# Performance work log

Hardware: AMD Instinct MI355X
Metric: run time of the kernel (lower is better)

## Reference

```python
import jax, jax.numpy as jnp
import numpy as np

B, S, D, H, DH, N, L, VOCAB = 8, 512, 1024, 16, 64, 32, 2, 128

def _ln(x, g, b, eps=1e-5):
    m = jnp.mean(x, axis=-1, keepdims=True)
    v = jnp.var(x, axis=-1, keepdims=True)
    return (x - m) * jax.lax.rsqrt(v + eps) * g + b

def setup_inputs() -> dict:
    key = jax.random.key(0)
    ks = jax.random.split(key, 10)
    std = 0.02
    inp = {
        "tokens": jax.random.randint(ks[0], (B, S), 0, VOCAB),
        "emb": jax.random.normal(ks[1], (VOCAB, D), jnp.float32) * std,
        "pos": jax.random.normal(ks[2], (1, S, D), jnp.float32) * std,
        "ln_g": jnp.ones((L, D), jnp.float32),
        "ln_b": jnp.zeros((L, D), jnp.float32),
        "wq": jax.random.normal(ks[3], (L, D, D), jnp.float32) * std,
        "bq": jnp.zeros((L, D), jnp.float32),
        "wk": jax.random.normal(ks[4], (L, D, D), jnp.float32) * std,
        "bk": jnp.zeros((L, D), jnp.float32),
        "wv": jax.random.normal(ks[5], (L, D, D), jnp.float32) * std,
        "bv": jnp.zeros((L, D), jnp.float32),
        "wg": jax.random.normal(ks[6], (L, D, D), jnp.float32) * std,
        "bg": jnp.zeros((L, D), jnp.float32),
        "wo": jax.random.normal(ks[7], (L, D, D), jnp.float32) * std,
        "bo": jnp.zeros((L, D), jnp.float32),
        "alpha_logit": jax.random.normal(ks[8], (L, H, N), jnp.float32) * 0.1,
        "fn_g": jnp.ones((D,), jnp.float32),
        "fn_b": jnp.zeros((D,), jnp.float32),
        "head_w": jax.random.normal(ks[9], (VOCAB, D), jnp.float32) * std,
        "head_b": jnp.zeros((VOCAB,), jnp.float32),
    }
    return inp

def _layer(x, g, b, Wq, Bq, Wk, Bk, Wv, Bv, Wg, Bg, Wo, Bo, alogit):
    residual = x
    xn = _ln(x, g, b)  # (B,S,D)
    def proj(W, Bb):
        return (jnp.einsum('bsd,ed->bse', xn, W) + Bb).reshape(x.shape[0], x.shape[1], H, DH)
    Q, K, V = proj(Wq, Bq), proj(Wk, Bk), proj(Wv, Bv)
    gate = jax.nn.silu(proj(Wg, Bg))
    alpha = jax.nn.sigmoid(alogit)  # (H,N)
    # scan over time; carry h: (B,H,N,DH)
    h0 = jnp.zeros((x.shape[0], H, N, DH), x.dtype)
    qkv = (jnp.moveaxis(Q, 1, 0), jnp.moveaxis(K, 1, 0), jnp.moveaxis(V, 1, 0))  # (S,B,H,DH)
    def step(h, qkv_t):
        q_t, k_t, v_t = qkv_t
        k_state = k_t[:, :, :N]  # state_dim <= d_head
        h = alpha[None, :, :, None] * h + jnp.einsum('bhi,bhj->bhij', k_state, v_t)
        q_state = q_t[:, :, :N]
        o_t = jnp.einsum('bhi,bhij->bhj', q_state, h)
        return h, o_t
    _, O = jax.lax.scan(step, h0, qkv)  # O: (S,B,H,DH)
    o = jnp.moveaxis(O, 0, 1) * gate  # (B,S,H,DH)
    o = o.reshape(x.shape[0], x.shape[1], H * DH)
    y = jnp.einsum('bsd,ed->bse', o, Wo) + Bo
    return residual + y

def reference(tokens, emb, pos, ln_g, ln_b, wq, bq, wk, bk, wv, bv, wg, bg, wo, bo,
              alpha_logit, fn_g, fn_b, head_w, head_b):
    x = emb[tokens] + pos[:, :tokens.shape[1], :]
    for l in range(L):
        x = _layer(x, ln_g[l], ln_b[l], wq[l], bq[l], wk[l], bk[l], wv[l], bv[l],
                   wg[l], bg[l], wo[l], bo[l], alpha_logit[l])
    x = _ln(x, fn_g, fn_b)
    logits = jnp.einsum('bsd,vd->bsv', x, head_w) + head_b
    return logits
```

## Files before the change

kernel.cpp:

```cpp
#include <hip/hip_runtime.h>
#include <hip/hip_bf16.h>
#include <stdint.h>

#define D_MODEL 1024
#define BB 8
#define SS 512
#define HH 16
#define DHH 64
#define NN 32
#define LL 2
#define VOC 128
#define M_TOK (BB * SS)
#define CHUNK 32
#define NCHUNK 16

typedef __bf16 bf16x8_t __attribute__((ext_vector_type(8)));
typedef float floatx4_t __attribute__((ext_vector_type(4)));
typedef unsigned short u16;

__device__ __forceinline__ float b2f(u16 u) {
  union { unsigned int i; float f; } c; c.i = ((unsigned int)u) << 16; return c.f;
}
__device__ __forceinline__ u16 f2b(float f) {
  union { float f; unsigned int i; } c; c.f = f;
  unsigned int r = c.i + 0x7fffu + ((c.i >> 16) & 1u);
  return (u16)(r >> 16);
}
__device__ __forceinline__ float sigm(float x) {
  return 1.0f / (1.0f + __expf(-x));
}

#define WSEG 524288
#define HSEG 32768
struct SrcP { const float* p[6]; };
__global__ __launch_bounds__(256) void k_f2b_all(
    SrcP src, u16* __restrict__ dst) {
  int i = blockIdx.x * 256 + threadIdx.x;
  int seg, within;
  if (i < 5 * WSEG) { seg = i / WSEG; within = i - seg * WSEG; }
  else { seg = 5; within = i - 5 * WSEG; if (within >= HSEG) return; }
  float4 v = ((const float4*)src.p[seg])[within];
  ushort4 o;
  o.x = f2b(v.x); o.y = f2b(v.y); o.z = f2b(v.z); o.w = f2b(v.w);
  ((ushort4*)dst)[(size_t)seg * WSEG + within] = o;
}

__global__ __launch_bounds__(256) void k_embed_ln(
    const int* __restrict__ tok, const float* __restrict__ emb,
    const float* __restrict__ pos, const float* __restrict__ g,
    const float* __restrict__ b, float* __restrict__ x, u16* __restrict__ xn) {
  int m = blockIdx.x;
  int s = m & (SS - 1);
  int tkn = tok[m];
  int t = threadIdx.x;
  int d = t * 4;
  float4 ev = *(const float4*)&emb[(size_t)tkn * D_MODEL + d];
  float4 pv = *(const float4*)&pos[(size_t)s * D_MODEL + d];
  float4 v;
  v.x = ev.x + pv.x; v.y = ev.y + pv.y; v.z = ev.z + pv.z; v.w = ev.w + pv.w;
  *(float4*)&x[(size_t)m * D_MODEL + d] = v;

  float s1 = v.x + v.y + v.z + v.w;
  float s2 = v.x * v.x + v.y * v.y + v.z * v.z + v.w * v.w;
#pragma unroll
  for (int o = 1; o < 64; o <<= 1) {
    s1 += __shfl_xor(s1, o);
    s2 += __shfl_xor(s2, o);
  }
  __shared__ float red[8];
  int wv = t >> 6, lane = t & 63;
  if (lane == 0) { red[wv] = s1; red[4 + wv] = s2; }
  __syncthreads();
  s1 = red[0] + red[1] + red[2] + red[3];
  s2 = red[4] + red[5] + red[6] + red[7];
  float mean = s1 * (1.0f / D_MODEL);
  float var = s2 * (1.0f / D_MODEL) - mean * mean;
  float rstd = rsqrtf(var + 1e-5f);
  float4 gv = *(const float4*)&g[d];
  float4 bv = *(const float4*)&b[d];
  ushort4 ov;
  ov.x = f2b((v.x - mean) * rstd * gv.x + bv.x);
  ov.y = f2b((v.y - mean) * rstd * gv.y + bv.y);
  ov.z = f2b((v.z - mean) * rstd * gv.z + bv.z);
  ov.w = f2b((v.w - mean) * rstd * gv.w + bv.w);
  *(ushort4*)&xn[(size_t)m * D_MODEL + d] = ov;
}

__global__ __launch_bounds__(256) void k_wo_ln(
    const float* __restrict__ P0, const float* __restrict__ P1,
    const float* __restrict__ bo, const float* __restrict__ g,
    const float* __restrict__ b, float* __restrict__ x, u16* __restrict__ xn) {
  int m = blockIdx.x;
  int t = threadIdx.x;
  size_t off = (size_t)m * D_MODEL + t * 4;
  float4 xv = *(const float4*)&x[off];
  float4 p0 = *(const float4*)&P0[off];
  float4 p1 = *(const float4*)&P1[off];
  float4 bb = *(const float4*)&bo[t * 4];
  float4 v;
  v.x = xv.x + p0.x + p1.x + bb.x;
  v.y = xv.y + p0.y + p1.y + bb.y;
  v.z = xv.z + p0.z + p1.z + bb.z;
  v.w = xv.w + p0.w + p1.w + bb.w;
  *(float4*)&x[off] = v;

  float s1 = v.x + v.y + v.z + v.w;
  float s2 = v.x * v.x + v.y * v.y + v.z * v.z + v.w * v.w;
#pragma unroll
  for (int o = 1; o < 64; o <<= 1) {
    s1 += __shfl_xor(s1, o);
    s2 += __shfl_xor(s2, o);
  }
  __shared__ float red[8];
  int wv = t >> 6, lane = t & 63;
  if (lane == 0) { red[wv] = s1; red[4 + wv] = s2; }
  __syncthreads();
  s1 = red[0] + red[1] + red[2] + red[3];
  s2 = red[4] + red[5] + red[6] + red[7];
  float mean = s1 * (1.0f / D_MODEL);
  float var = s2 * (1.0f / D_MODEL) - mean * mean;
  float rstd = rsqrtf(var + 1e-5f);
  float4 gv = *(const float4*)&g[t * 4];
  float4 bv = *(const float4*)&b[t * 4];
  ushort4 ov;
  ov.x = f2b((v.x - mean) * rstd * gv.x + bv.x);
  ov.y = f2b((v.y - mean) * rstd * gv.y + bv.y);
  ov.z = f2b((v.z - mean) * rstd * gv.z + bv.z);
  ov.w = f2b((v.w - mean) * rstd * gv.w + bv.w);
  *(ushort4*)&xn[off] = ov;
}

__global__ __launch_bounds__(256) void k_head_red(
    const float* __restrict__ Ph, const float* __restrict__ hb,
    float* __restrict__ out) {
  int i4 = blockIdx.x * 256 + threadIdx.x;
  float4 s = ((const float4*)hb)[i4 & 31];
#pragma unroll
  for (int z = 0; z < 8; ++z) {
    float4 p = ((const float4*)(Ph + (size_t)z * M_TOK * VOC))[i4];
    s.x += p.x; s.y += p.y; s.z += p.z; s.w += p.w;
  }
  ((float4*)out)[i4] = s;
}

struct Task { const u16* W; const float* bias; void* out; };
struct Tasks { Task t[4]; };

__device__ __forceinline__ void async_cp16(const void* g, void* l) {
  __builtin_amdgcn_global_load_lds(
      (const __attribute__((address_space(1))) void*)g,
      (__attribute__((address_space(3))) void*)l, 16, 0, 0);
}

template <int EPI>
__global__ __launch_bounds__(256) void k_gemm(
    const u16* __restrict__ A, Tasks tasks, int N, int K, int kspan,
    size_t pstride) {
  __shared__ u16 ldsA[128 * 64];
  __shared__ u16 ldsB[128 * 64];
  const int tid = threadIdx.x;
  const int lane = tid & 63, wv = tid >> 6;
  const int bm = blockIdx.x * 128, bn = blockIdx.y * 128;
  const Task tk = tasks.t[EPI == 4 ? 0 : blockIdx.z];
  const u16* W = tk.W;
  const int kb = (EPI == 4) ? blockIdx.z * kspan : 0;
  const int ke = kb + kspan;

  const int wm = (wv >> 1) * 64, wn = (wv & 1) * 64;
  floatx4_t acc[4][4];
#pragma unroll
  for (int i = 0; i < 4; ++i)
#pragma unroll
    for (int j = 0; j < 4; ++j)
#pragma unroll
      for (int r = 0; r < 4; ++r) acc[i][j][r] = 0.0f;

  const int srow = lane >> 3;
  const int sk8 = (lane & 7) ^ srow;

  for (int k0 = kb; k0 < ke; k0 += 64) {
#pragma unroll
    for (int c = 0; c < 4; ++c) {
      int chunk = wv * 4 + c;
      const u16* ga = A + (size_t)(bm + chunk * 8 + srow) * K + (k0 + sk8 * 8);
      async_cp16(ga, &ldsA[chunk * 512]);
      const u16* gb = W + (size_t)(bn + chunk * 8 + srow) * K + (k0 + sk8 * 8);
      async_cp16(gb, &ldsB[chunk * 512]);
    }
    __syncthreads();
#pragma unroll
    for (int kt = 0; kt < 2; ++kt) {
      const int k8 = kt * 4 + (lane >> 4);
      bf16x8_t af[4], bfr[4];
#pragma unroll
      for (int mi = 0; mi < 4; ++mi) {
        int row = wm + mi * 16 + (lane & 15);
        int gran = row * 8 + (k8 ^ (row & 7));
        af[mi] = *(const bf16x8_t*)&ldsA[gran * 8];
      }
#pragma unroll
      for (int ni = 0; ni < 4; ++ni) {
        int row = wn + ni * 16 + (lane & 15);
        int gran = row * 8 + (k8 ^ (row & 7));
        bfr[ni] = *(const bf16x8_t*)&ldsB[gran * 8];
      }
#pragma unroll
      for (int mi = 0; mi < 4; ++mi)
#pragma unroll
        for (int ni = 0; ni < 4; ++ni)
          acc[mi][ni] = __builtin_amdgcn_mfma_f32_16x16x32_bf16(
              af[mi], bfr[ni], acc[mi][ni], 0, 0, 0);
    }
    __syncthreads();
  }

  float* outp4 = (EPI == 4)
      ? (float*)tk.out + (size_t)blockIdx.z * pstride : nullptr;
#pragma unroll
  for (int ni = 0; ni < 4; ++ni) {
    int col = bn + wn + ni * 16 + (lane & 15);
    float bias = (EPI == 2) ? tk.bias[col] : 0.0f;
#pragma unroll
    for (int mi = 0; mi < 4; ++mi) {
      int row0 = bm + wm + mi * 16 + (lane >> 4) * 4;
#pragma unroll
      for (int r = 0; r < 4; ++r) {
        size_t idx = (size_t)(row0 + r) * N + col;
        float v = acc[mi][ni][r] + bias;
        if (EPI == 2) ((u16*)tk.out)[idx] = f2b(v);
        else          outp4[idx] = v;
      }
    }
  }
}

__global__ __launch_bounds__(128) void k_scan_a(
    const u16* __restrict__ K, const u16* __restrict__ V,
    const float* __restrict__ alog, float* __restrict__ Hc) {
  int blk = blockIdx.x;
  int bh = blk >> 4;
  int c = blk & (NCHUNK - 1);
  int b = bh >> 4, h = bh & 15;
  int t = threadIdx.x;
  int jl = t & 31, ig = t >> 5;
  int i0 = ig * 8, j0 = jl * 2;

  __shared__ float kl[CHUNK][32];
  __shared__ float vl[CHUNK][64];

  size_t base = (size_t)b * SS * 1024 + h * 64 + (size_t)c * CHUNK * 1024;
  const u16* kb = K + base;
  const u16* vb = V + base;
  for (int idx = t; idx < CHUNK * 32; idx += 128) {
    int s = idx >> 5, i = idx & 31;
    kl[s][i] = b2f(kb[(size_t)s * 1024 + i]);
  }
  for (int idx = t; idx < CHUNK * 64; idx += 128) {
    int s = idx >> 6, j = idx & 63;
    vl[s][j] = b2f(vb[(size_t)s * 1024 + j]);
  }
  __syncthreads();

  float al[8];
#pragma unroll
  for (int u = 0; u < 8; ++u) al[u] = sigm(alog[h * NN + i0 + u]);

  float hr[8][2];
#pragma unroll
  for (int u = 0; u < 8; ++u) { hr[u][0] = 0.f; hr[u][1] = 0.f; }

  for (int s = 0; s < CHUNK; ++s) {
    float4 kA = *(const float4*)&kl[s][i0];
    float4 kB = *(const float4*)&kl[s][i0 + 4];
    float2 vv = *(const float2*)&vl[s][j0];
    float kc[8] = {kA.x, kA.y, kA.z, kA.w, kB.x, kB.y, kB.z, kB.w};
#pragma unroll
    for (int u = 0; u < 8; ++u) {
      hr[u][0] = al[u] * hr[u][0] + kc[u] * vv.x;
      hr[u][1] = al[u] * hr[u][1] + kc[u] * vv.y;
    }
  }
  float* out = Hc + (size_t)blk * 2048;
#pragma unroll
  for (int u = 0; u < 8; ++u) {
    float2 w = make_float2(hr[u][0], hr[u][1]);
    *(float2*)&out[(i0 + u) * 64 + j0] = w;
  }
}

__global__ __launch_bounds__(256) void k_scan_b(
    const float* __restrict__ alog, float* __restrict__ Hc) {
  int bh = blockIdx.x >> 3;
  int ij = ((blockIdx.x & 7) << 8) + threadIdx.x;
  int h = bh & 15;
  int i = ij >> 6;
  float a = sigm(alog[h * NN + i]);
  float a2 = a * a, a4 = a2 * a2, a8 = a4 * a4, a16 = a8 * a8;
  float aC = a16 * a16;
  float carry = 0.f;
  float* p = Hc + (size_t)bh * NCHUNK * 2048 + ij;
#pragma unroll 4
  for (int c = 0; c < NCHUNK; ++c) {
    float tmp = p[(size_t)c * 2048];
    p[(size_t)c * 2048] = carry;
    carry = aC * carry + tmp;
  }
}

__global__ __launch_bounds__(128) void k_scan_c(
    const u16* __restrict__ Q, const u16* __restrict__ K,
    const u16* __restrict__ V, const u16* __restrict__ G,
    const float* __restrict__ alog, const float* __restrict__ Hc,
    u16* __restrict__ og) {
  int blk = blockIdx.x;
  int bh = blk >> 4;
  int c = blk & (NCHUNK - 1);
  int b = bh >> 4, h = bh & 15;
  int t = threadIdx.x;
  int jl = t & 31, ig = t >> 5;
  int i0 = ig * 8, j0 = jl * 2;

  __shared__ u16 ql[CHUNK][32];
  __shared__ u16 kl[CHUNK][32];
  __shared__ u16 vl[CHUNK][64];
  __shared__ u16 gl[CHUNK][64];
  __shared__ float po[4][CHUNK][64];

  size_t base = (size_t)b * SS * 1024 + h * 64 + (size_t)c * CHUNK * 1024;
  const u16* qb = Q + base;
  const u16* kb = K + base;
  const u16* vb = V + base;
  const u16* gb = G + base;
  for (int idx = t; idx < CHUNK * 32; idx += 128) {
    int s = idx >> 5, i = idx & 31;
    ql[s][i] = qb[(size_t)s * 1024 + i];
    kl[s][i] = kb[(size_t)s * 1024 + i];
  }
  for (int idx = t; idx < CHUNK * 64; idx += 128) {
    int s = idx >> 6, j = idx & 63;
    vl[s][j] = vb[(size_t)s * 1024 + j];
    gl[s][j] = gb[(size_t)s * 1024 + j];
  }
  __syncthreads();

  float al[8];
#pragma unroll
  for (int u = 0; u < 8; ++u) al[u] = sigm(alog[h * NN + i0 + u]);

  const float* hin = Hc + (size_t)blk * 2048;
  float hr[8][2];
#pragma unroll
  for (int u = 0; u < 8; ++u) {
    float2 w = *(const float2*)&hin[(i0 + u) * 64 + j0];
    hr[u][0] = w.x; hr[u][1] = w.y;
  }

  for (int s = 0; s < CHUNK; ++s) {
    ushort4 kA = *(const ushort4*)&kl[s][i0];
    ushort4 kB = *(const ushort4*)&kl[s][i0 + 4];
    ushort4 qA = *(const ushort4*)&ql[s][i0];
    ushort4 qB = *(const ushort4*)&ql[s][i0 + 4];
    u16 v0 = vl[s][j0], v1 = vl[s][j0 + 1];
    float kc[8] = {b2f(kA.x), b2f(kA.y), b2f(kA.z), b2f(kA.w),
                   b2f(kB.x), b2f(kB.y), b2f(kB.z), b2f(kB.w)};
    float qc[8] = {b2f(qA.x), b2f(qA.y), b2f(qA.z), b2f(qA.w),
                   b2f(qB.x), b2f(qB.y), b2f(qB.z), b2f(qB.w)};
    float vx = b2f(v0), vy = b2f(v1);
    float p0 = 0.f, p1 = 0.f;
#pragma unroll
    for (int u = 0; u < 8; ++u) {
      float h0 = al[u] * hr[u][0] + kc[u] * vx;
      float h1 = al[u] * hr[u][1] + kc[u] * vy;
      hr[u][0] = h0; hr[u][1] = h1;
      p0 += qc[u] * h0;
      p1 += qc[u] * h1;
    }
    *(float2*)&po[ig][s][j0] = make_float2(p0, p1);
  }
  __syncthreads();

  for (int idx = t; idx < CHUNK * 64; idx += 128) {
    int s = idx >> 6, j = idx & 63;
    float o = po[0][s][j] + po[1][s][j] + po[2][s][j] + po[3][s][j];
    float gg = b2f(gl[s][j]);
    float sg = gg * sigm(gg);
    og[((size_t)b * SS + c * CHUNK + s) * 1024 + h * 64 + j] = f2b(o * sg);
  }
}

extern "C" void kernel_launch(void* const* d_in, const int* in_sizes, int n_in,
                              void* d_out, int out_size, void* d_ws, size_t ws_size,
                              hipStream_t stream) {
  const int*   tok  = (const int*)d_in[0];
  const float* emb  = (const float*)d_in[1];
  const float* pos  = (const float*)d_in[2];
  const float* ln_g = (const float*)d_in[3];
  const float* ln_b = (const float*)d_in[4];
  const float* wq   = (const float*)d_in[5];
  const float* bq   = (const float*)d_in[6];
  const float* wk   = (const float*)d_in[7];
  const float* bk   = (const float*)d_in[8];
  const float* wv   = (const float*)d_in[9];
  const float* bv   = (const float*)d_in[10];
  const float* wg   = (const float*)d_in[11];
  const float* bg   = (const float*)d_in[12];
  const float* wo   = (const float*)d_in[13];
  const float* bo   = (const float*)d_in[14];
  const float* alog = (const float*)d_in[15];
  const float* fn_g = (const float*)d_in[16];
  const float* fn_b = (const float*)d_in[17];
  const float* hw   = (const float*)d_in[18];
  const float* hb   = (const float*)d_in[19];

  char* ws = (char*)d_ws;
  float* x   = (float*)(ws);
  u16*   xn  = (u16*)(ws + (size_t)(16 << 20));
  u16*   qb  = (u16*)(ws + (size_t)(24 << 20));
  u16*   kb  = (u16*)(ws + (size_t)(32 << 20));
  u16*   vb  = (u16*)(ws + (size_t)(40 << 20));
  u16*   gb  = (u16*)(ws + (size_t)(48 << 20));
  float* Hc  = (float*)(ws + (size_t)(56 << 20));
  u16*   wB  = (u16*)(ws + (size_t)(72 << 20));
  u16* wqB = wB;
  u16* wkB = wB + (size_t)2 * 1024 * 1024;
  u16* wvB = wB + (size_t)4 * 1024 * 1024;
  u16* wgB = wB + (size_t)6 * 1024 * 1024;
  u16* woB = wB + (size_t)8 * 1024 * 1024;
  u16* hwB = wB + (size_t)10 * 1024 * 1024;
  float* P0 = (float*)(ws + (size_t)(24 << 20));
  float* P1 = (float*)(ws + (size_t)(40 << 20));
  float* Ph = Hc;

  SrcP sp; sp.p[0] = wq; sp.p[1] = wk; sp.p[2] = wv; sp.p[3] = wg; sp.p[4] = wo; sp.p[5] = hw;
  const int TOT4 = 5 * WSEG + HSEG;
  k_f2b_all<<<(TOT4 + 255) / 256, 256, 0, stream>>>(sp, wB);

  k_embed_ln<<<M_TOK, 256, 0, stream>>>(tok, emb, pos, ln_g, ln_b, x, xn);

  for (int l = 0; l < LL; ++l) {
    Tasks tq;
    tq.t[0] = Task{wqB + (size_t)l * D_MODEL * D_MODEL, bq + l * D_MODEL, (void*)qb};
    tq.t[1] = Task{wkB + (size_t)l * D_MODEL * D_MODEL, bk + l * D_MODEL, (void*)kb};
    tq.t[2] = Task{wvB + (size_t)l * D_MODEL * D_MODEL, bv + l * D_MODEL, (void*)vb};
    tq.t[3] = Task{wgB + (size_t)l * D_MODEL * D_MODEL, bg + l * D_MODEL, (void*)gb};
    k_gemm<2><<<dim3(32, 8, 4), 256, 0, stream>>>(xn, tq, D_MODEL, D_MODEL,
                                                  D_MODEL, 0);

    const float* al = alog + l * HH * NN;
    k_scan_a<<<128 * NCHUNK, 128, 0, stream>>>(kb, vb, al, Hc);
    k_scan_b<<<128 * 8, 256, 0, stream>>>(al, Hc);
    k_scan_c<<<128 * NCHUNK, 128, 0, stream>>>(qb, kb, vb, gb, al, Hc, xn);

    Tasks to;
    to.t[0] = Task{woB + (size_t)l * D_MODEL * D_MODEL, bo + l * D_MODEL, (void*)P0};
    to.t[1] = to.t[0]; to.t[2] = to.t[0]; to.t[3] = to.t[0];
    k_gemm<4><<<dim3(32, 8, 2), 256, 0, stream>>>(xn, to, D_MODEL, D_MODEL,
                                                  512, (size_t)M_TOK * D_MODEL);

    const float* ng = (l + 1 < LL) ? ln_g + (l + 1) * D_MODEL : fn_g;
    const float* nb = (l + 1 < LL) ? ln_b + (l + 1) * D_MODEL : fn_b;
    k_wo_ln<<<M_TOK, 256, 0, stream>>>(P0, P1, bo + l * D_MODEL, ng, nb, x, xn);
  }

  Tasks th;
  th.t[0] = Task{hwB, hb, (void*)Ph};
  th.t[1] = th.t[0]; th.t[2] = th.t[0]; th.t[3] = th.t[0];
  k_gemm<4><<<dim3(32, 1, 8), 256, 0, stream>>>(xn, th, VOC, D_MODEL,
                                                128, (size_t)M_TOK * VOC);
  k_head_red<<<512, 256, 0, stream>>>(Ph, hb, (float*)d_out);
}
```

Measured before the change: 399.1 us.

## Store split-K partials in bf16, vectorize scan loads, halve scan_c reduction buffer

Split-K partial outputs of the Wo and head GEMMs are written and read as bf16 instead of fp32, which halves that traffic but adds rounding error before the partials are summed. The scan kernels now load K/V/Q/G with 16-byte vector loads instead of scalar loads. scan_c folds half of its partial sums with a cross-lane shuffle, so the LDS buffer shrinks to two slices and the gated output is written as ushort2 pairs. The scan_b carry loop is fully unrolled.

```diff
diff --git a/kernel.cpp b/kernel.cpp
--- a/kernel.cpp
+++ b/kernel.cpp
@@ -17,6 +17,7 @@
 typedef __bf16 bf16x8_t __attribute__((ext_vector_type(8)));
 typedef float floatx4_t __attribute__((ext_vector_type(4)));
 typedef unsigned short u16;
+typedef unsigned short u16x8 __attribute__((ext_vector_type(8)));
 
 __device__ __forceinline__ float b2f(u16 u) {
   union { unsigned int i; float f; } c; c.i = ((unsigned int)u) << 16; return c.f;
@@ -87,21 +88,21 @@
 }
 
 __global__ __launch_bounds__(256) void k_wo_ln(
-    const float* __restrict__ P0, const float* __restrict__ P1,
+    const u16* __restrict__ P0, const u16* __restrict__ P1,
     const float* __restrict__ bo, const float* __restrict__ g,
     const float* __restrict__ b, float* __restrict__ x, u16* __restrict__ xn) {
   int m = blockIdx.x;
   int t = threadIdx.x;
   size_t off = (size_t)m * D_MODEL + t * 4;
   float4 xv = *(const float4*)&x[off];
-  float4 p0 = *(const float4*)&P0[off];
-  float4 p1 = *(const float4*)&P1[off];
+  ushort4 p0 = *(const ushort4*)&P0[off];
+  ushort4 p1 = *(const ushort4*)&P1[off];
   float4 bb = *(const float4*)&bo[t * 4];
   float4 v;
-  v.x = xv.x + p0.x + p1.x + bb.x;
-  v.y = xv.y + p0.y + p1.y + bb.y;
-  v.z = xv.z + p0.z + p1.z + bb.z;
-  v.w = xv.w + p0.w + p1.w + bb.w;
+  v.x = xv.x + b2f(p0.x) + b2f(p1.x) + bb.x;
+  v.y = xv.y + b2f(p0.y) + b2f(p1.y) + bb.y;
+  v.z = xv.z + b2f(p0.z) + b2f(p1.z) + bb.z;
+  v.w = xv.w + b2f(p0.w) + b2f(p1.w) + bb.w;
   *(float4*)&x[off] = v;
 
   float s1 = v.x + v.y + v.z + v.w;
@@ -131,14 +132,14 @@
 }
 
 __global__ __launch_bounds__(256) void k_head_red(
-    const float* __restrict__ Ph, const float* __restrict__ hb,
+    const u16* __restrict__ Ph, const float* __restrict__ hb,
     float* __restrict__ out) {
   int i4 = blockIdx.x * 256 + threadIdx.x;
   float4 s = ((const float4*)hb)[i4 & 31];
 #pragma unroll
   for (int z = 0; z < 8; ++z) {
-    float4 p = ((const float4*)(Ph + (size_t)z * M_TOK * VOC))[i4];
-    s.x += p.x; s.y += p.y; s.z += p.z; s.w += p.w;
+    ushort4 p = *(const ushort4*)&Ph[(size_t)z * M_TOK * VOC + (size_t)i4 * 4];
+    s.x += b2f(p.x); s.y += b2f(p.y); s.z += b2f(p.z); s.w += b2f(p.w);
   }
   ((float4*)out)[i4] = s;
 }
@@ -161,9 +162,9 @@
   const int tid = threadIdx.x;
   const int lane = tid & 63, wv = tid >> 6;
   const int bm = blockIdx.x * 128, bn = blockIdx.y * 128;
-  const Task tk = tasks.t[EPI == 4 ? 0 : blockIdx.z];
+  const Task tk = tasks.t[EPI == 5 ? 0 : blockIdx.z];
   const u16* W = tk.W;
-  const int kb = (EPI == 4) ? blockIdx.z * kspan : 0;
+  const int kb = (EPI == 5) ? blockIdx.z * kspan : 0;
   const int ke = kb + kspan;
 
   const int wm = (wv >> 1) * 64, wn = (wv & 1) * 64;
@@ -214,8 +215,8 @@
     __syncthreads();
   }
 
-  float* outp4 = (EPI == 4)
-      ? (float*)tk.out + (size_t)blockIdx.z * pstride : nullptr;
+  u16* outp16 = (EPI == 5)
+      ? (u16*)tk.out + (size_t)blockIdx.z * pstride : (u16*)tk.out;
 #pragma unroll
   for (int ni = 0; ni < 4; ++ni) {
     int col = bn + wn + ni * 16 + (lane & 15);
@@ -226,9 +227,7 @@
 #pragma unroll
       for (int r = 0; r < 4; ++r) {
         size_t idx = (size_t)(row0 + r) * N + col;
-        float v = acc[mi][ni][r] + bias;
-        if (EPI == 2) ((u16*)tk.out)[idx] = f2b(v);
-        else          outp4[idx] = v;
+        outp16[idx] = f2b(acc[mi][ni][r] + bias);
       }
     }
   }
@@ -251,13 +250,19 @@
   size_t base = (size_t)b * SS * 1024 + h * 64 + (size_t)c * CHUNK * 1024;
   const u16* kb = K + base;
   const u16* vb = V + base;
-  for (int idx = t; idx < CHUNK * 32; idx += 128) {
-    int s = idx >> 5, i = idx & 31;
-    kl[s][i] = b2f(kb[(size_t)s * 1024 + i]);
-  }
-  for (int idx = t; idx < CHUNK * 64; idx += 128) {
-    int s = idx >> 6, j = idx & 63;
-    vl[s][j] = b2f(vb[(size_t)s * 1024 + j]);
+  {
+    int s = t >> 2, e = (t & 3) * 8;
+    u16x8 kv = *(const u16x8*)&kb[(size_t)s * 1024 + e];
+#pragma unroll
+    for (int u = 0; u < 8; ++u) kl[s][e + u] = b2f(kv[u]);
+  }
+#pragma unroll
+  for (int r = 0; r < 2; ++r) {
+    int idx = t + r * 128;
+    int s = idx >> 3, e = (idx & 7) * 8;
+    u16x8 vv = *(const u16x8*)&vb[(size_t)s * 1024 + e];
+#pragma unroll
+    for (int u = 0; u < 8; ++u) vl[s][e + u] = b2f(vv[u]);
   }
   __syncthreads();
 
@@ -299,7 +304,7 @@
   float aC = a16 * a16;
   float carry = 0.f;
   float* p = Hc + (size_t)bh * NCHUNK * 2048 + ij;
-#pragma unroll 4
+#pragma unroll
   for (int c = 0; c < NCHUNK; ++c) {
     float tmp = p[(size_t)c * 2048];
     p[(size_t)c * 2048] = carry;
@@ -324,22 +329,24 @@
   __shared__ u16 kl[CHUNK][32];
   __shared__ u16 vl[CHUNK][64];
   __shared__ u16 gl[CHUNK][64];
-  __shared__ float po[4][CHUNK][64];
+  __shared__ float po[2][CHUNK][64];
 
   size_t base = (size_t)b * SS * 1024 + h * 64 + (size_t)c * CHUNK * 1024;
   const u16* qb = Q + base;
   const u16* kb = K + base;
   const u16* vb = V + base;
   const u16* gb = G + base;
-  for (int idx = t; idx < CHUNK * 32; idx += 128) {
-    int s = idx >> 5, i = idx & 31;
-    ql[s][i] = qb[(size_t)s * 1024 + i];
-    kl[s][i] = kb[(size_t)s * 1024 + i];
-  }
-  for (int idx = t; idx < CHUNK * 64; idx += 128) {
-    int s = idx >> 6, j = idx & 63;
-    vl[s][j] = vb[(size_t)s * 1024 + j];
-    gl[s][j] = gb[(size_t)s * 1024 + j];
+  {
+    int s = t >> 2, e = (t & 3) * 8;
+    *(u16x8*)&ql[s][e] = *(const u16x8*)&qb[(size_t)s * 1024 + e];
+    *(u16x8*)&kl[s][e] = *(const u16x8*)&kb[(size_t)s * 1024 + e];
+  }
+#pragma unroll
+  for (int r = 0; r < 2; ++r) {
+    int idx = t + r * 128;
+    int s = idx >> 3, e = (idx & 7) * 8;
+    *(u16x8*)&vl[s][e] = *(const u16x8*)&vb[(size_t)s * 1024 + e];
+    *(u16x8*)&gl[s][e] = *(const u16x8*)&gb[(size_t)s * 1024 + e];
   }
   __syncthreads();
 
@@ -375,16 +382,23 @@
       p0 += qc[u] * h0;
       p1 += qc[u] * h1;
     }
-    *(float2*)&po[ig][s][j0] = make_float2(p0, p1);
+    p0 += __shfl_xor(p0, 32);
+    p1 += __shfl_xor(p1, 32);
+    if (!(t & 32)) *(float2*)&po[t >> 6][s][j0] = make_float2(p0, p1);
   }
   __syncthreads();
 
-  for (int idx = t; idx < CHUNK * 64; idx += 128) {
-    int s = idx >> 6, j = idx & 63;
-    float o = po[0][s][j] + po[1][s][j] + po[2][s][j] + po[3][s][j];
-    float gg = b2f(gl[s][j]);
-    float sg = gg * sigm(gg);
-    og[((size_t)b * SS + c * CHUNK + s) * 1024 + h * 64 + j] = f2b(o * sg);
+#pragma unroll
+  for (int r = 0; r < 8; ++r) {
+    int idx = t + r * 128;
+    int s = idx >> 5, jp = (idx & 31) * 2;
+    float o0 = po[0][s][jp] + po[1][s][jp];
+    float o1 = po[0][s][jp + 1] + po[1][s][jp + 1];
+    float g0 = b2f(gl[s][jp]), g1 = b2f(gl[s][jp + 1]);
+    ushort2 st;
+    st.x = f2b(o0 * g0 * sigm(g0));
+    st.y = f2b(o1 * g1 * sigm(g1));
+    *(ushort2*)&og[((size_t)b * SS + c * CHUNK + s) * 1024 + h * 64 + jp] = st;
   }
 }
 
@@ -427,9 +441,9 @@
   u16* wgB = wB + (size_t)6 * 1024 * 1024;
   u16* woB = wB + (size_t)8 * 1024 * 1024;
   u16* hwB = wB + (size_t)10 * 1024 * 1024;
-  float* P0 = (float*)(ws + (size_t)(24 << 20));
-  float* P1 = (float*)(ws + (size_t)(40 << 20));
-  float* Ph = Hc;
+  u16* P0 = (u16*)(ws + (size_t)(24 << 20));
+  u16* P1 = (u16*)(ws + (size_t)(32 << 20));
+  u16* Ph = (u16*)(ws + (size_t)(56 << 20));
 
   SrcP sp; sp.p[0] = wq; sp.p[1] = wk; sp.p[2] = wv; sp.p[3] = wg; sp.p[4] = wo; sp.p[5] = hw;
   const int TOT4 = 5 * WSEG + HSEG;
@@ -454,7 +468,7 @@
     Tasks to;
     to.t[0] = Task{woB + (size_t)l * D_MODEL * D_MODEL, bo + l * D_MODEL, (void*)P0};
     to.t[1] = to.t[0]; to.t[2] = to.t[0]; to.t[3] = to.t[0];
-    k_gemm<4><<<dim3(32, 8, 2), 256, 0, stream>>>(xn, to, D_MODEL, D_MODEL,
+    k_gemm<5><<<dim3(32, 8, 2), 256, 0, stream>>>(xn, to, D_MODEL, D_MODEL,
                                                   512, (size_t)M_TOK * D_MODEL);
 
     const float* ng = (l + 1 < LL) ? ln_g + (l + 1) * D_MODEL : fn_g;
@@ -465,7 +479,7 @@
   Tasks th;
   th.t[0] = Task{hwB, hb, (void*)Ph};
   th.t[1] = th.t[0]; th.t[2] = th.t[0]; th.t[3] = th.t[0];
-  k_gemm<4><<<dim3(32, 1, 8), 256, 0, stream>>>(xn, th, VOC, D_MODEL,
+  k_gemm<5><<<dim3(32, 1, 8), 256, 0, stream>>>(xn, th, VOC, D_MODEL,
                                                 128, (size_t)M_TOK * VOC);
   k_head_red<<<512, 256, 0, stream>>>(Ph, hb, (float*)d_out);
 }
```

Measured after the change: 377.2 us. 1.06x faster.
